# Performance work log

Measured on AMD Instinct MI355X. Metric: run time of the kernel, lower is better.

Reference implementation:

```python
import jax, jax.numpy as jnp
import numpy as np

T, B, H = 512, 128, 512


def setup_inputs() -> dict:
    key = jax.random.key(0)
    k1, k2, k3, k4 = jax.random.split(key, 4)
    scale_i = 1.0 / np.sqrt(H)
    return {
        "ins": jax.random.normal(k1, (T, B, H), dtype=jnp.float32),
        "resets": jax.random.randint(k2, (T, B), 0, 2).astype(bool),
        "h0": jnp.zeros((B, H), dtype=jnp.float32),
        "W_i": jax.random.normal(k3, (H, 3 * H), dtype=jnp.float32) * scale_i,
        "b_i": jnp.zeros((3 * H,), dtype=jnp.float32),
        "W_h": jax.random.normal(k4, (H, 3 * H), dtype=jnp.float32) * scale_i,
        "b_hn": jnp.zeros((H,), dtype=jnp.float32),
    }


def reference(ins, resets, h0, W_i, b_i, W_h, b_hn):
    # Precompute all input-side gate projections in one big GEMM: [T,B,3H]
    gi = jnp.einsum('tbh,hk->tbk', ins, W_i) + b_i

    def step(h, inp):
        gi_t, r_t = inp  # gi_t: [B,3H], r_t: [B] bool
        # episode reset -> zero carry (flax initialize_carry default is zeros)
        h = jnp.where(r_t[:, None], 0.0, h)
        gh = h @ W_h  # [B,3H]
        ir, iz, inn = jnp.split(gi_t, 3, axis=-1)
        hr, hz, hn = jnp.split(gh, 3, axis=-1)
        r = jax.nn.sigmoid(ir + hr)
        z = jax.nn.sigmoid(iz + hz)
        n = jnp.tanh(inn + r * (hn + b_hn))
        new_h = (1.0 - z) * n + z * h
        return new_h, new_h

    final_h, ys = jax.lax.scan(step, h0, (gi, resets))
    return final_h, ys  # carry [B,H], outputs [T,B,H]
```

## Files before the change

### kernel.cpp

```cpp
#include <hip/hip_runtime.h>
#include <stdint.h>
#include <math.h>

#define T_DIM 512
#define B_DIM 128
#define H_DIM 512
#define K_MAX_SWEEP 32

typedef _Float16 half8 __attribute__((ext_vector_type(8)));
typedef float    f32x4 __attribute__((ext_vector_type(4)));

__global__ void k_weights(const float* __restrict__ Wi, const float* __restrict__ Wh,
                          _Float16* __restrict__ Bsw) {
    __shared__ float sh[32][33];
    int nt = blockIdx.x;
    int kt = blockIdx.y;
    int m  = blockIdx.z;
    const float* W = m ? Wh : Wi;
    int ty = threadIdx.x >> 5, tx = threadIdx.x & 31;
    for (int i = 0; i < 4; ++i) {
        int r = ty + i * 8;
        sh[r][tx] = W[(kt * 32 + r) * 1536 + nt * 32 + tx];
    }
    __syncthreads();
    for (int i = 0; i < 4; ++i) {
        int nloc  = ty + i * 8;
        int nglob = nt * 32 + nloc;
        float v   = sh[tx][nloc];
        int kglob = kt * 32 + tx;
        int np, kp;
        if (m == 0) { np = nglob;                                  kp = kglob;       }
        else        { np = (nglob < 1024) ? nglob : nglob + 512;   kp = 512 + kglob; }
        Bsw[np * 1024 + kp] = (_Float16)v;
    }
}

__global__ void k_xcast(const float* __restrict__ ins, _Float16* __restrict__ Acomb) {
    size_t i   = (size_t)blockIdx.x * blockDim.x + threadIdx.x;
    size_t row = i >> 6;
    int    c8  = (int)(i & 63);
    const float4* s = (const float4*)(ins + row * 512 + c8 * 8);
    float4 a = s[0], b = s[1];
    half8 hv;
    hv[0] = (_Float16)a.x; hv[1] = (_Float16)a.y; hv[2] = (_Float16)a.z; hv[3] = (_Float16)a.w;
    hv[4] = (_Float16)b.x; hv[5] = (_Float16)b.y; hv[6] = (_Float16)b.z; hv[7] = (_Float16)b.w;
    *(half8*)(Acomb + row * 1024 + c8 * 8) = hv;
}

__global__ void k_age(const uint8_t* __restrict__ resets, uint16_t* __restrict__ age,
                      int* __restrict__ hist2d) {
    int b = blockIdx.x;
    int t = threadIdx.x;
    __shared__ int sAny;
    __shared__ int sh[512];
    __shared__ int hist[512];
    if (t == 0) sAny = 0;
    hist[t] = 0;
    __syncthreads();
    if ((t & 3) && resets[t]) atomicOr(&sAny, 1);
    __syncthreads();
    bool is_i32 = (sAny == 0);
    int idx = t * B_DIM + b;
    int r;
    if (is_i32) r = (((const int*)resets)[idx] != 0);
    else        r = (resets[idx] != 0);
    sh[t] = r ? t : 0;
    __syncthreads();
    for (int off = 1; off < 512; off <<= 1) {
        int v = (t >= off) ? sh[t - off] : 0;
        __syncthreads();
        if (v > sh[t]) sh[t] = v;
        __syncthreads();
    }
    int a = t - sh[t];
    age[idx] = (uint16_t)a;
    atomicAdd(&hist[a], 1);
    __syncthreads();
    hist2d[b * 512 + t] = hist[t];
}

__global__ void k_prefix(const int* __restrict__ hist2d, int* __restrict__ cnt,
                         int* __restrict__ offs, int* __restrict__ cur) {
    int a = threadIdx.x;
    int s = 0;
    for (int b = 0; b < 128; ++b) s += hist2d[b * 512 + a];
    __shared__ int sh[512];
    sh[a] = s;
    __syncthreads();
    for (int off = 1; off < 512; off <<= 1) {
        int v = (a >= off) ? sh[a - off] : 0;
        __syncthreads();
        sh[a] += v;
        __syncthreads();
    }
    cnt[a]  = s;
    offs[a] = sh[a] - s;
    cur[a]  = sh[a] - s;
}

__global__ void k_scatter(const uint16_t* __restrict__ age, int* __restrict__ cur,
                          int* __restrict__ rows) {
    int b = blockIdx.x;
    int t = threadIdx.x;
    __shared__ int lcnt[512];
    __shared__ int lbase[512];
    lcnt[t] = 0;
    __syncthreads();
    int a  = age[t * B_DIM + b];
    int li = atomicAdd(&lcnt[a], 1);
    __syncthreads();
    if (lcnt[t] > 0) lbase[t] = atomicAdd(&cur[t], lcnt[t]);
    __syncthreads();
    rows[lbase[a] + li] = t * B_DIM + b;
}

template <bool F16A>
__launch_bounds__(256, 4)
__global__ void k_sweep(const float* __restrict__ ins, const _Float16* __restrict__ Bsw,
                        _Float16* __restrict__ Acomb, const int* __restrict__ rows,
                        const int* __restrict__ cnt, const int* __restrict__ offs,
                        const float* __restrict__ b_i, const float* __restrict__ b_hn,
                        float* __restrict__ out, int sweep) {
    int nrows    = cnt[sweep];
    int tileBase = blockIdx.y * 128;
    if (tileBase >= nrows) return;
    int cgi  = blockIdx.x;
    int off0 = offs[sweep];
    float* ys = out + B_DIM * H_DIM;

    __shared__ int rowsL[128];
    __shared__ __align__(16) _Float16 As[128][64];
    __shared__ __align__(16) _Float16 Bs[3][32][64];

    int tid = threadIdx.x;
    if (tid < 128) {
        int gi = tileBase + tid;
        rowsL[tid] = rows[off0 + ((gi < nrows) ? gi : 0)];
    }
    __syncthreads();

    f32x4 acc[2][8];
    for (int i = 0; i < 2; ++i)
        for (int j = 0; j < 8; ++j) acc[i][j] = (f32x4){0.f, 0.f, 0.f, 0.f};

    const int kIters = (sweep == 0) ? 8 : 16;
    int w = tid >> 6, lane = tid & 63, q = lane >> 4, l15 = lane & 15;
    int w32 = w * 32;
    int lr = tid >> 1, c0 = (tid & 1) * 4, rs = lr & 7;
    int brow = tid >> 3, bch = tid & 7, brs = brow & 7;
    int la = l15 & 7;

    for (int it = 0; it < kIters; ++it) {
        int  kw    = it * 64;
        bool xpart = (kw < 512);
        if (F16A) {
            const uint4* s = (const uint4*)(Acomb + (size_t)rowsL[lr] * 1024 + kw + c0 * 8);
            uint4 v0 = s[0], v1 = s[1], v2 = s[2], v3 = s[3];
            *(uint4*)&As[lr][((c0 + 0) ^ rs) << 3] = v0;
            *(uint4*)&As[lr][((c0 + 1) ^ rs) << 3] = v1;
            *(uint4*)&As[lr][((c0 + 2) ^ rs) << 3] = v2;
            *(uint4*)&As[lr][((c0 + 3) ^ rs) << 3] = v3;
        } else {
            int rowidx = rowsL[lr];
            const float* src = xpart ? (ins + (size_t)rowidx * 512 + kw)
                                     : (ys + (size_t)(rowidx - 128) * 512 + (kw - 512));
            const float4* s4 = (const float4*)(src + c0 * 8);
            float4 v[8];
            #pragma unroll
            for (int j = 0; j < 8; ++j) v[j] = s4[j];
            #pragma unroll
            for (int c = 0; c < 4; ++c) {
                float4 a = v[c * 2], b2 = v[c * 2 + 1];
                half8 hv;
                hv[0] = (_Float16)a.x;  hv[1] = (_Float16)a.y;
                hv[2] = (_Float16)a.z;  hv[3] = (_Float16)a.w;
                hv[4] = (_Float16)b2.x; hv[5] = (_Float16)b2.y;
                hv[6] = (_Float16)b2.z; hv[7] = (_Float16)b2.w;
                *(half8*)&As[lr][((c0 + c) ^ rs) << 3] = hv;
            }
        }
        {
            int nbs[3];
            nbs[0] = cgi * 32;
            nbs[1] = 512 + cgi * 32;
            nbs[2] = (xpart ? 1024 : 1536) + cgi * 32;
            #pragma unroll
            for (int s = 0; s < 3; ++s) {
                const uint4* g = (const uint4*)(Bsw + (nbs[s] + brow) * 1024 + kw + bch * 8);
                *(uint4*)&Bs[s][brow][(bch ^ brs) << 3] = *g;
            }
        }
        __syncthreads();
        #pragma unroll
        for (int ks = 0; ks < 2; ++ks) {
            int ca = ks * 4 + q;
            int sc = (ca ^ la) << 3;
            half8 a0  = *(const half8*)&As[w32 + l15][sc];
            half8 a1  = *(const half8*)&As[w32 + 16 + l15][sc];
            half8 b00 = *(const half8*)&Bs[0][l15][sc];
            half8 b01 = *(const half8*)&Bs[0][16 + l15][sc];
            half8 b10 = *(const half8*)&Bs[1][l15][sc];
            half8 b11 = *(const half8*)&Bs[1][16 + l15][sc];
            half8 b20 = *(const half8*)&Bs[2][l15][sc];
            half8 b21 = *(const half8*)&Bs[2][16 + l15][sc];
            acc[0][0] = __builtin_amdgcn_mfma_f32_16x16x32_f16(a0, b00, acc[0][0], 0, 0, 0);
            acc[1][0] = __builtin_amdgcn_mfma_f32_16x16x32_f16(a1, b00, acc[1][0], 0, 0, 0);
            acc[0][1] = __builtin_amdgcn_mfma_f32_16x16x32_f16(a0, b01, acc[0][1], 0, 0, 0);
            acc[1][1] = __builtin_amdgcn_mfma_f32_16x16x32_f16(a1, b01, acc[1][1], 0, 0, 0);
            acc[0][2] = __builtin_amdgcn_mfma_f32_16x16x32_f16(a0, b10, acc[0][2], 0, 0, 0);
            acc[1][2] = __builtin_amdgcn_mfma_f32_16x16x32_f16(a1, b10, acc[1][2], 0, 0, 0);
            acc[0][3] = __builtin_amdgcn_mfma_f32_16x16x32_f16(a0, b11, acc[0][3], 0, 0, 0);
            acc[1][3] = __builtin_amdgcn_mfma_f32_16x16x32_f16(a1, b11, acc[1][3], 0, 0, 0);
            if (xpart) {
                acc[0][4] = __builtin_amdgcn_mfma_f32_16x16x32_f16(a0, b20, acc[0][4], 0, 0, 0);
                acc[1][4] = __builtin_amdgcn_mfma_f32_16x16x32_f16(a1, b20, acc[1][4], 0, 0, 0);
                acc[0][5] = __builtin_amdgcn_mfma_f32_16x16x32_f16(a0, b21, acc[0][5], 0, 0, 0);
                acc[1][5] = __builtin_amdgcn_mfma_f32_16x16x32_f16(a1, b21, acc[1][5], 0, 0, 0);
            } else {
                acc[0][6] = __builtin_amdgcn_mfma_f32_16x16x32_f16(a0, b20, acc[0][6], 0, 0, 0);
                acc[1][6] = __builtin_amdgcn_mfma_f32_16x16x32_f16(a1, b20, acc[1][6], 0, 0, 0);
                acc[0][7] = __builtin_amdgcn_mfma_f32_16x16x32_f16(a0, b21, acc[0][7], 0, 0, 0);
                acc[1][7] = __builtin_amdgcn_mfma_f32_16x16x32_f16(a1, b21, acc[1][7], 0, 0, 0);
            }
        }
        __syncthreads();
    }

    #pragma unroll
    for (int tm = 0; tm < 2; ++tm) {
        int lrow_base = w32 + tm * 16 + q * 4;
        #pragma unroll
        for (int reg = 0; reg < 4; ++reg) {
            int lrow = lrow_base + reg;
            if (tileBase + lrow >= nrows) continue;
            int rowidx = rowsL[lrow];
            int t = rowidx >> 7, b = rowidx & 127;
            #pragma unroll
            for (int hf = 0; hf < 2; ++hf) {
                int gj = cgi * 32 + hf * 16 + l15;
                float rpre = acc[tm][0 + hf][reg] + b_i[gj];
                float zpre = acc[tm][2 + hf][reg] + b_i[512 + gj];
                float innv = acc[tm][4 + hf][reg] + b_i[1024 + gj];
                float hnv  = acc[tm][6 + hf][reg];
                float r = 1.f / (1.f + __expf(-rpre));
                float z = 1.f / (1.f + __expf(-zpre));
                float n = tanhf(innv + r * (hnv + b_hn[gj]));
                float hprev = (sweep > 0) ? ys[(size_t)(rowidx - 128) * 512 + gj] : 0.f;
                float hnew  = (1.f - z) * n + z * hprev;
                ys[(size_t)rowidx * 512 + gj] = hnew;
                if (F16A && rowidx + 128 < T_DIM * B_DIM)
                    Acomb[(size_t)(rowidx + 128) * 1024 + 512 + gj] = (_Float16)hnew;
                if (t == T_DIM - 1) out[b * 512 + gj] = hnew;
            }
        }
    }
}

__global__ void k_cleanup(const float* __restrict__ ins, const _Float16* __restrict__ Bsw,
                          const int* __restrict__ rows, const int* __restrict__ cnt,
                          const int* __restrict__ offs, const float* __restrict__ b_i,
                          const float* __restrict__ b_hn, float* __restrict__ out) {
    float* ys = out + B_DIM * H_DIM;
    __shared__ float xs[512], hs[512];
    int j = threadIdx.x;
    for (int a = K_MAX_SWEEP; a < 512; ++a) {
        int n = cnt[a];
        if (n == 0) return;
        int o = offs[a];
        for (int i = 0; i < n; ++i) {
            int rowidx = rows[o + i];
            xs[j] = ins[rowidx * 512 + j];
            hs[j] = ys[(rowidx - 128) * 512 + j];
            __syncthreads();
            float rpre = b_i[j], zpre = b_i[512 + j], innv = b_i[1024 + j], hnv = 0.f;
            for (int k = 0; k < 512; ++k) {
                float xk = xs[k], hk = hs[k];
                rpre += xk * (float)Bsw[j * 1024 + k]          + hk * (float)Bsw[j * 1024 + 512 + k];
                zpre += xk * (float)Bsw[(512 + j) * 1024 + k]  + hk * (float)Bsw[(512 + j) * 1024 + 512 + k];
                innv += xk * (float)Bsw[(1024 + j) * 1024 + k];
                hnv  += hk * (float)Bsw[(1536 + j) * 1024 + 512 + k];
            }
            float r  = 1.f / (1.f + __expf(-rpre));
            float z  = 1.f / (1.f + __expf(-zpre));
            float nn = tanhf(innv + r * (hnv + b_hn[j]));
            float hnew = (1.f - z) * nn + z * hs[j];
            ys[rowidx * 512 + j] = hnew;
            int t = rowidx >> 7, b = rowidx & 127;
            if (t == 511) out[b * 512 + j] = hnew;
            __syncthreads();
        }
    }
}

extern "C" void kernel_launch(void* const* d_in, const int* in_sizes, int n_in,
                              void* d_out, int out_size, void* d_ws, size_t ws_size,
                              hipStream_t stream) {
    const float*   ins    = (const float*)d_in[0];
    const uint8_t* resets = (const uint8_t*)d_in[1];
    const float*   Wi     = (const float*)d_in[3];
    const float*   b_i    = (const float*)d_in[4];
    const float*   Wh     = (const float*)d_in[5];
    const float*   b_hn   = (const float*)d_in[6];
    float*         out    = (float*)d_out;

    const size_t BSW_B   = 2048ull * 1024 * 2;
    const size_t ACOMB_B = 65536ull * 1024 * 2;
    const size_t TAIL_B  = 131072 + 262144 + 3 * 2048 + 262144;
    char* ws = (char*)d_ws;
    size_t off = 0;
    _Float16* Bsw = (_Float16*)(ws + off); off += BSW_B;
    bool big = (ws_size >= BSW_B + ACOMB_B + TAIL_B);
    _Float16* Acomb = nullptr;
    if (big) { Acomb = (_Float16*)(ws + off); off += ACOMB_B; }
    uint16_t* age    = (uint16_t*)(ws + off); off += 131072;
    int*      hist2d = (int*)(ws + off);      off += 262144;
    int*      cnt    = (int*)(ws + off);      off += 2048;
    int*      offs   = (int*)(ws + off);      off += 2048;
    int*      cur    = (int*)(ws + off);      off += 2048;
    int*      rows   = (int*)(ws + off);      off += 262144;

    k_weights<<<dim3(48, 16, 2), dim3(256), 0, stream>>>(Wi, Wh, Bsw);
    if (big)
        k_xcast<<<dim3(16384), dim3(256), 0, stream>>>(ins, Acomb);
    k_age    <<<dim3(128), dim3(512), 0, stream>>>(resets, age, hist2d);
    k_prefix <<<dim3(1),   dim3(512), 0, stream>>>(hist2d, cnt, offs, cur);
    k_scatter<<<dim3(128), dim3(512), 0, stream>>>(age, cur, rows);

    for (int k = 0; k < K_MAX_SWEEP; ++k) {
        int tiles = 512 / (k + 1) + 1;
        if (tiles > 512) tiles = 512;
        if (big)
            k_sweep<true><<<dim3(16, tiles), dim3(256), 0, stream>>>(ins, Bsw, Acomb, rows, cnt,
                                                                     offs, b_i, b_hn, out, k);
        else
            k_sweep<false><<<dim3(16, tiles), dim3(256), 0, stream>>>(ins, Bsw, Acomb, rows, cnt,
                                                                      offs, b_i, b_hn, out, k);
    }
    k_cleanup<<<dim3(1), dim3(512), 0, stream>>>(ins, Bsw, rows, cnt, offs, b_i, b_hn, out);
}
```

Before: 936.9 us.

## Replace per-sweep launches and serial cleanup with persistent grid-barrier tail kernel

Only the first three age sweeps now get their own kernel launches. All later ages, including the former single-block serial cleanup for ages of 32 and above, are handled by one persistent kernel of 512 blocks. That kernel loops over ages, splits each age's tiles across its blocks, and separates ages with an atomic grid-wide barrier. This removes many small launches and the slow serial cleanup, but it relies on all 512 blocks being resident at once and pays a barrier cost for every remaining age.

```diff
diff --git a/kernel.cpp b/kernel.cpp
--- a/kernel.cpp
+++ b/kernel.cpp
@@ -5,7 +5,8 @@
 #define T_DIM 512
 #define B_DIM 128
 #define H_DIM 512
-#define K_MAX_SWEEP 32
+#define KSTART_TAIL 3
+#define TOTAL_ROWS (T_DIM * B_DIM)
 
 typedef _Float16 half8 __attribute__((ext_vector_type(8)));
 typedef float    f32x4 __attribute__((ext_vector_type(4)));
@@ -80,8 +81,10 @@
 }
 
 __global__ void k_prefix(const int* __restrict__ hist2d, int* __restrict__ cnt,
-                         int* __restrict__ offs, int* __restrict__ cur) {
+                         int* __restrict__ offs, int* __restrict__ cur,
+                         int* __restrict__ bar) {
     int a = threadIdx.x;
+    if (a == 0) bar[0] = 0;
     int s = 0;
     for (int b = 0; b < 128; ++b) s += hist2d[b * 512 + a];
     __shared__ int sh[512];
@@ -115,24 +118,16 @@
 }
 
 template <bool F16A>
-__launch_bounds__(256, 4)
-__global__ void k_sweep(const float* __restrict__ ins, const _Float16* __restrict__ Bsw,
-                        _Float16* __restrict__ Acomb, const int* __restrict__ rows,
-                        const int* __restrict__ cnt, const int* __restrict__ offs,
-                        const float* __restrict__ b_i, const float* __restrict__ b_hn,
-                        float* __restrict__ out, int sweep) {
-    int nrows    = cnt[sweep];
-    int tileBase = blockIdx.y * 128;
-    if (tileBase >= nrows) return;
-    int cgi  = blockIdx.x;
-    int off0 = offs[sweep];
-    float* ys = out + B_DIM * H_DIM;
-
-    __shared__ int rowsL[128];
-    __shared__ __align__(16) _Float16 As[128][64];
-    __shared__ __align__(16) _Float16 Bs[3][32][64];
-
+__device__ __forceinline__ void sweep_tile(
+    int sweep, int cgi, int tileBase, int nrows, int off0,
+    const float* __restrict__ ins, const _Float16* __restrict__ Bsw,
+    _Float16* __restrict__ Acomb, const int* __restrict__ rows,
+    const float* __restrict__ b_i, const float* __restrict__ b_hn,
+    float* __restrict__ out, float* __restrict__ ys,
+    int (&rowsL)[128], _Float16 (&As)[128][64], _Float16 (&Bs)[3][32][64])
+{
     int tid = threadIdx.x;
+    __syncthreads();
     if (tid < 128) {
         int gi = tileBase + tid;
         rowsL[tid] = rows[off0 + ((gi < nrows) ? gi : 0)];
@@ -248,7 +243,7 @@
                 float hprev = (sweep > 0) ? ys[(size_t)(rowidx - 128) * 512 + gj] : 0.f;
                 float hnew  = (1.f - z) * n + z * hprev;
                 ys[(size_t)rowidx * 512 + gj] = hnew;
-                if (F16A && rowidx + 128 < T_DIM * B_DIM)
+                if (F16A && rowidx + 128 < TOTAL_ROWS)
                     Acomb[(size_t)(rowidx + 128) * 1024 + 512 + gj] = (_Float16)hnew;
                 if (t == T_DIM - 1) out[b * 512 + gj] = hnew;
             }
@@ -256,39 +251,64 @@
     }
 }
 
-__global__ void k_cleanup(const float* __restrict__ ins, const _Float16* __restrict__ Bsw,
-                          const int* __restrict__ rows, const int* __restrict__ cnt,
-                          const int* __restrict__ offs, const float* __restrict__ b_i,
-                          const float* __restrict__ b_hn, float* __restrict__ out) {
+template <bool F16A>
+__launch_bounds__(256, 4)
+__global__ void k_sweep(const float* __restrict__ ins, const _Float16* __restrict__ Bsw,
+                        _Float16* __restrict__ Acomb, const int* __restrict__ rows,
+                        const int* __restrict__ cnt, const int* __restrict__ offs,
+                        const float* __restrict__ b_i, const float* __restrict__ b_hn,
+                        float* __restrict__ out, int sweep) {
+    int nrows    = cnt[sweep];
+    int tileBase = blockIdx.y * 128;
+    if (tileBase >= nrows) return;
+    __shared__ int rowsL[128];
+    __shared__ __align__(16) _Float16 As[128][64];
+    __shared__ __align__(16) _Float16 Bs[3][32][64];
     float* ys = out + B_DIM * H_DIM;
-    __shared__ float xs[512], hs[512];
-    int j = threadIdx.x;
-    for (int a = K_MAX_SWEEP; a < 512; ++a) {
-        int n = cnt[a];
-        if (n == 0) return;
-        int o = offs[a];
-        for (int i = 0; i < n; ++i) {
-            int rowidx = rows[o + i];
-            xs[j] = ins[rowidx * 512 + j];
-            hs[j] = ys[(rowidx - 128) * 512 + j];
-            __syncthreads();
-            float rpre = b_i[j], zpre = b_i[512 + j], innv = b_i[1024 + j], hnv = 0.f;
-            for (int k = 0; k < 512; ++k) {
-                float xk = xs[k], hk = hs[k];
-                rpre += xk * (float)Bsw[j * 1024 + k]          + hk * (float)Bsw[j * 1024 + 512 + k];
-                zpre += xk * (float)Bsw[(512 + j) * 1024 + k]  + hk * (float)Bsw[(512 + j) * 1024 + 512 + k];
-                innv += xk * (float)Bsw[(1024 + j) * 1024 + k];
-                hnv  += hk * (float)Bsw[(1536 + j) * 1024 + 512 + k];
-            }
-            float r  = 1.f / (1.f + __expf(-rpre));
-            float z  = 1.f / (1.f + __expf(-zpre));
-            float nn = tanhf(innv + r * (hnv + b_hn[j]));
-            float hnew = (1.f - z) * nn + z * hs[j];
-            ys[rowidx * 512 + j] = hnew;
-            int t = rowidx >> 7, b = rowidx & 127;
-            if (t == 511) out[b * 512 + j] = hnew;
-            __syncthreads();
-        }
+    sweep_tile<F16A>(sweep, blockIdx.x, tileBase, nrows, offs[sweep],
+                     ins, Bsw, Acomb, rows, b_i, b_hn, out, ys, rowsL, As, Bs);
+}
+
+template <bool F16A>
+__launch_bounds__(256, 4)
+__global__ void k_tail(const float* __restrict__ ins, const _Float16* __restrict__ Bsw,
+                       _Float16* __restrict__ Acomb, const int* __restrict__ rows,
+                       const int* __restrict__ cnt, const int* __restrict__ offs,
+                       const float* __restrict__ b_i, const float* __restrict__ b_hn,
+                       float* __restrict__ out, int kstart, int* bar) {
+    __shared__ int rowsL[128];
+    __shared__ __align__(16) _Float16 As[128][64];
+    __shared__ __align__(16) _Float16 Bs[3][32][64];
+    float* ys = out + B_DIM * H_DIM;
+    int tid = threadIdx.x;
+    int phase = 0;
+    const int nblk = (int)gridDim.x;
+
+    for (int k = kstart; k < 512; ++k) {
+        int done = offs[k];
+        if (done >= TOTAL_ROWS) break;
+        int nrows = cnt[k];
+        if (nrows > 0) {
+            int nwork = (((nrows + 127) >> 7) << 4);
+            for (int wi = blockIdx.x; wi < nwork; wi += nblk) {
+                int cgi = wi & 15;
+                int tb  = (wi >> 4) << 7;
+                sweep_tile<F16A>(k, cgi, tb, nrows, done,
+                                 ins, Bsw, Acomb, rows, b_i, b_hn, out, ys,
+                                 rowsL, As, Bs);
+            }
+        }
+        ++phase;
+        __syncthreads();
+        if (tid == 0) {
+            __threadfence();
+            __hip_atomic_fetch_add(bar, 1, __ATOMIC_RELEASE, __HIP_MEMORY_SCOPE_AGENT);
+            while (__hip_atomic_load(bar, __ATOMIC_ACQUIRE, __HIP_MEMORY_SCOPE_AGENT)
+                   < phase * nblk) {
+                __builtin_amdgcn_s_sleep(2);
+            }
+        }
+        __syncthreads();
     }
 }
 
@@ -305,7 +325,7 @@
 
     const size_t BSW_B   = 2048ull * 1024 * 2;
     const size_t ACOMB_B = 65536ull * 1024 * 2;
-    const size_t TAIL_B  = 131072 + 262144 + 3 * 2048 + 262144;
+    const size_t TAIL_B  = 131072 + 262144 + 3 * 2048 + 262144 + 64;
     char* ws = (char*)d_ws;
     size_t off = 0;
     _Float16* Bsw = (_Float16*)(ws + off); off += BSW_B;
@@ -318,15 +338,16 @@
     int*      offs   = (int*)(ws + off);      off += 2048;
     int*      cur    = (int*)(ws + off);      off += 2048;
     int*      rows   = (int*)(ws + off);      off += 262144;
+    int*      bar    = (int*)(ws + off);      off += 64;
 
     k_weights<<<dim3(48, 16, 2), dim3(256), 0, stream>>>(Wi, Wh, Bsw);
     if (big)
         k_xcast<<<dim3(16384), dim3(256), 0, stream>>>(ins, Acomb);
     k_age    <<<dim3(128), dim3(512), 0, stream>>>(resets, age, hist2d);
-    k_prefix <<<dim3(1),   dim3(512), 0, stream>>>(hist2d, cnt, offs, cur);
+    k_prefix <<<dim3(1),   dim3(512), 0, stream>>>(hist2d, cnt, offs, cur, bar);
     k_scatter<<<dim3(128), dim3(512), 0, stream>>>(age, cur, rows);
 
-    for (int k = 0; k < K_MAX_SWEEP; ++k) {
+    for (int k = 0; k < KSTART_TAIL; ++k) {
         int tiles = 512 / (k + 1) + 1;
         if (tiles > 512) tiles = 512;
         if (big)
@@ -336,5 +357,10 @@
             k_sweep<false><<<dim3(16, tiles), dim3(256), 0, stream>>>(ins, Bsw, Acomb, rows, cnt,
                                                                       offs, b_i, b_hn, out, k);
     }
-    k_cleanup<<<dim3(1), dim3(512), 0, stream>>>(ins, Bsw, rows, cnt, offs, b_i, b_hn, out);
-}
+    if (big)
+        k_tail<true><<<dim3(512), dim3(256), 0, stream>>>(ins, Bsw, Acomb, rows, cnt, offs,
+                                                          b_i, b_hn, out, KSTART_TAIL, bar);
+    else
+        k_tail<false><<<dim3(512), dim3(256), 0, stream>>>(ins, Bsw, Acomb, rows, cnt, offs,
+                                                           b_i, b_hn, out, KSTART_TAIL, bar);
+}
```

After: 2.825 ms. +201.5%, slower.

## Precompute input gates in one GEMM and run tail sweeps in a persistent kernel

Applied to the files above, without the earlier changes.

Adds k_gi, which computes all input-side gate projections in one full GEMM over every row. It finishes age-0 rows directly and stores the other rows' gate pre-activations as fp16 in a new gi2 buffer. Each sweep then only multiplies against W_h, with K halved. Sweeps from age 3 onward run in a single persistent 256-block kernel that uses an atomic grid barrier between ages, replacing the per-age launches and the serial single-block cleanup. This needs a large extra workspace, adds a spin-barrier that assumes all blocks are co-resident, and rounds the gate pre-activations to fp16.

```diff
diff --git a/kernel.cpp b/kernel.cpp
--- a/kernel.cpp
+++ b/kernel.cpp
@@ -5,7 +5,9 @@
 #define T_DIM 512
 #define B_DIM 128
 #define H_DIM 512
+#define KSTART_TAIL 3
 #define K_MAX_SWEEP 32
+#define TOTAL_ROWS (T_DIM * B_DIM)
 
 typedef _Float16 half8 __attribute__((ext_vector_type(8)));
 typedef float    f32x4 __attribute__((ext_vector_type(4)));
@@ -80,8 +82,10 @@
 }
 
 __global__ void k_prefix(const int* __restrict__ hist2d, int* __restrict__ cnt,
-                         int* __restrict__ offs, int* __restrict__ cur) {
+                         int* __restrict__ offs, int* __restrict__ cur,
+                         int* __restrict__ bar) {
     int a = threadIdx.x;
+    if (a == 0) bar[0] = 0;
     int s = 0;
     for (int b = 0; b < 128; ++b) s += hist2d[b * 512 + a];
     __shared__ int sh[512];
@@ -112,6 +116,253 @@
     if (lcnt[t] > 0) lbase[t] = atomicAdd(&cur[t], lcnt[t]);
     __syncthreads();
     rows[lbase[a] + li] = t * B_DIM + b;
+}
+
+
+__launch_bounds__(256, 4)
+__global__ void k_gi(const _Float16* __restrict__ AcombC, _Float16* __restrict__ Acomb,
+                     const _Float16* __restrict__ Bsw, const uint16_t* __restrict__ age,
+                     const float* __restrict__ b_i, const float* __restrict__ b_hn,
+                     float* __restrict__ out, _Float16* __restrict__ gi2) {
+    int cgi     = blockIdx.x;
+    int rowbase = blockIdx.y * 128;
+    float* ys = out + B_DIM * H_DIM;
+
+    __shared__ __align__(16) _Float16 As[128][64];
+    __shared__ __align__(16) _Float16 Bs[3][32][64];
+
+    int tid = threadIdx.x;
+    f32x4 acc[2][6];
+    for (int i = 0; i < 2; ++i)
+        for (int j = 0; j < 6; ++j) acc[i][j] = (f32x4){0.f, 0.f, 0.f, 0.f};
+
+    int w = tid >> 6, lane = tid & 63, q = lane >> 4, l15 = lane & 15;
+    int w32 = w * 32;
+    int lr = tid >> 1, c0 = (tid & 1) * 4, rs = lr & 7;
+    int brow = tid >> 3, bch = tid & 7, brs = brow & 7;
+    int la = l15 & 7;
+
+    for (int it = 0; it < 8; ++it) {
+        int kw = it * 64;
+        {
+            const uint4* s = (const uint4*)(AcombC + (size_t)(rowbase + lr) * 1024 + kw + c0 * 8);
+            uint4 v0 = s[0], v1 = s[1], v2 = s[2], v3 = s[3];
+            *(uint4*)&As[lr][((c0 + 0) ^ rs) << 3] = v0;
+            *(uint4*)&As[lr][((c0 + 1) ^ rs) << 3] = v1;
+            *(uint4*)&As[lr][((c0 + 2) ^ rs) << 3] = v2;
+            *(uint4*)&As[lr][((c0 + 3) ^ rs) << 3] = v3;
+        }
+        {
+            int nbs[3] = { cgi * 32, 512 + cgi * 32, 1024 + cgi * 32 };
+            #pragma unroll
+            for (int s = 0; s < 3; ++s) {
+                const uint4* g = (const uint4*)(Bsw + (nbs[s] + brow) * 1024 + kw + bch * 8);
+                *(uint4*)&Bs[s][brow][(bch ^ brs) << 3] = *g;
+            }
+        }
+        __syncthreads();
+        #pragma unroll
+        for (int ks = 0; ks < 2; ++ks) {
+            int ca = ks * 4 + q;
+            int sc = (ca ^ la) << 3;
+            half8 a0 = *(const half8*)&As[w32 + l15][sc];
+            half8 a1 = *(const half8*)&As[w32 + 16 + l15][sc];
+            #pragma unroll
+            for (int s = 0; s < 3; ++s) {
+                half8 b0 = *(const half8*)&Bs[s][l15][sc];
+                half8 b1 = *(const half8*)&Bs[s][16 + l15][sc];
+                acc[0][s*2+0] = __builtin_amdgcn_mfma_f32_16x16x32_f16(a0, b0, acc[0][s*2+0], 0, 0, 0);
+                acc[1][s*2+0] = __builtin_amdgcn_mfma_f32_16x16x32_f16(a1, b0, acc[1][s*2+0], 0, 0, 0);
+                acc[0][s*2+1] = __builtin_amdgcn_mfma_f32_16x16x32_f16(a0, b1, acc[0][s*2+1], 0, 0, 0);
+                acc[1][s*2+1] = __builtin_amdgcn_mfma_f32_16x16x32_f16(a1, b1, acc[1][s*2+1], 0, 0, 0);
+            }
+        }
+        __syncthreads();
+    }
+
+    #pragma unroll
+    for (int tm = 0; tm < 2; ++tm) {
+        #pragma unroll
+        for (int reg = 0; reg < 4; ++reg) {
+            int lrow = w32 + tm * 16 + q * 4 + reg;
+            int row  = rowbase + lrow;
+            int t = row >> 7, b = row & 127;
+            int a = age[row];
+            #pragma unroll
+            for (int hf = 0; hf < 2; ++hf) {
+                int gj = cgi * 32 + hf * 16 + l15;
+                float rpre = acc[tm][0 + hf][reg] + b_i[gj];
+                float zpre = acc[tm][2 + hf][reg] + b_i[512 + gj];
+                float innv = acc[tm][4 + hf][reg] + b_i[1024 + gj];
+                if (a == 0) {
+                    float r = 1.f / (1.f + __expf(-rpre));
+                    float z = 1.f / (1.f + __expf(-zpre));
+                    float n = tanhf(innv + r * b_hn[gj]);
+                    float hnew = (1.f - z) * n;
+                    ys[(size_t)row * 512 + gj] = hnew;
+                    if (row + 128 < TOTAL_ROWS)
+                        Acomb[(size_t)(row + 128) * 1024 + 512 + gj] = (_Float16)hnew;
+                    if (t == T_DIM - 1) out[b * 512 + gj] = hnew;
+                } else {
+                    size_t gb = ((size_t)cgi * TOTAL_ROWS + row) * 96 + hf * 16 + l15;
+                    gi2[gb]      = (_Float16)rpre;
+                    gi2[gb + 32] = (_Float16)zpre;
+                    gi2[gb + 64] = (_Float16)innv;
+                }
+            }
+        }
+    }
+}
+
+__device__ __forceinline__ void sweep_h_tile(
+    int cgi, int tileBase, int nrows, int off0,
+    _Float16* __restrict__ Acomb, const _Float16* __restrict__ Bsw,
+    const int* __restrict__ rows, const _Float16* __restrict__ gi2,
+    const float* __restrict__ b_hn, float* __restrict__ out, float* __restrict__ ys,
+    int (&rowsL)[128], _Float16 (&As)[128][64], _Float16 (&Bs)[3][32][64])
+{
+    int tid = threadIdx.x;
+    __syncthreads();
+    if (tid < 128) {
+        int gi = tileBase + tid;
+        rowsL[tid] = rows[off0 + ((gi < nrows) ? gi : 0)];
+    }
+    __syncthreads();
+
+    f32x4 acc[2][6];
+    for (int i = 0; i < 2; ++i)
+        for (int j = 0; j < 6; ++j) acc[i][j] = (f32x4){0.f, 0.f, 0.f, 0.f};
+
+    int w = tid >> 6, lane = tid & 63, q = lane >> 4, l15 = lane & 15;
+    int w32 = w * 32;
+    int lr = tid >> 1, c0 = (tid & 1) * 4, rs = lr & 7;
+    int brow = tid >> 3, bch = tid & 7, brs = brow & 7;
+    int la = l15 & 7;
+
+    for (int it = 0; it < 8; ++it) {
+        int kw = it * 64;
+        {
+            const uint4* s = (const uint4*)(Acomb + (size_t)rowsL[lr] * 1024 + 512 + kw + c0 * 8);
+            uint4 v0 = s[0], v1 = s[1], v2 = s[2], v3 = s[3];
+            *(uint4*)&As[lr][((c0 + 0) ^ rs) << 3] = v0;
+            *(uint4*)&As[lr][((c0 + 1) ^ rs) << 3] = v1;
+            *(uint4*)&As[lr][((c0 + 2) ^ rs) << 3] = v2;
+            *(uint4*)&As[lr][((c0 + 3) ^ rs) << 3] = v3;
+        }
+        {
+            int nbs[3] = { cgi * 32, 512 + cgi * 32, 1536 + cgi * 32 };
+            #pragma unroll
+            for (int s = 0; s < 3; ++s) {
+                const uint4* g = (const uint4*)(Bsw + (nbs[s] + brow) * 1024 + 512 + kw + bch * 8);
+                *(uint4*)&Bs[s][brow][(bch ^ brs) << 3] = *g;
+            }
+        }
+        __syncthreads();
+        #pragma unroll
+        for (int ks = 0; ks < 2; ++ks) {
+            int ca = ks * 4 + q;
+            int sc = (ca ^ la) << 3;
+            half8 a0 = *(const half8*)&As[w32 + l15][sc];
+            half8 a1 = *(const half8*)&As[w32 + 16 + l15][sc];
+            #pragma unroll
+            for (int s = 0; s < 3; ++s) {
+                half8 b0 = *(const half8*)&Bs[s][l15][sc];
+                half8 b1 = *(const half8*)&Bs[s][16 + l15][sc];
+                acc[0][s*2+0] = __builtin_amdgcn_mfma_f32_16x16x32_f16(a0, b0, acc[0][s*2+0], 0, 0, 0);
+                acc[1][s*2+0] = __builtin_amdgcn_mfma_f32_16x16x32_f16(a1, b0, acc[1][s*2+0], 0, 0, 0);
+                acc[0][s*2+1] = __builtin_amdgcn_mfma_f32_16x16x32_f16(a0, b1, acc[0][s*2+1], 0, 0, 0);
+                acc[1][s*2+1] = __builtin_amdgcn_mfma_f32_16x16x32_f16(a1, b1, acc[1][s*2+1], 0, 0, 0);
+            }
+        }
+        __syncthreads();
+    }
+
+    #pragma unroll
+    for (int tm = 0; tm < 2; ++tm) {
+        #pragma unroll
+        for (int reg = 0; reg < 4; ++reg) {
+            int lrow = w32 + tm * 16 + q * 4 + reg;
+            if (tileBase + lrow >= nrows) continue;
+            int row = rowsL[lrow];
+            int t = row >> 7, b = row & 127;
+            #pragma unroll
+            for (int hf = 0; hf < 2; ++hf) {
+                int gj = cgi * 32 + hf * 16 + l15;
+                size_t gb = ((size_t)cgi * TOTAL_ROWS + row) * 96 + hf * 16 + l15;
+                float gr  = (float)gi2[gb];
+                float gz  = (float)gi2[gb + 32];
+                float gin = (float)gi2[gb + 64];
+                float rpre = acc[tm][0 + hf][reg] + gr;
+                float zpre = acc[tm][2 + hf][reg] + gz;
+                float r = 1.f / (1.f + __expf(-rpre));
+                float z = 1.f / (1.f + __expf(-zpre));
+                float n = tanhf(gin + r * (acc[tm][4 + hf][reg] + b_hn[gj]));
+                float hprev = ys[(size_t)(row - 128) * 512 + gj];
+                float hnew  = (1.f - z) * n + z * hprev;
+                ys[(size_t)row * 512 + gj] = hnew;
+                if (row + 128 < TOTAL_ROWS)
+                    Acomb[(size_t)(row + 128) * 1024 + 512 + gj] = (_Float16)hnew;
+                if (t == T_DIM - 1) out[b * 512 + gj] = hnew;
+            }
+        }
+    }
+}
+
+__launch_bounds__(256, 4)
+__global__ void k_sweep_h(_Float16* __restrict__ Acomb, const _Float16* __restrict__ Bsw,
+                          const int* __restrict__ rows, const int* __restrict__ cnt,
+                          const int* __restrict__ offs, const _Float16* __restrict__ gi2,
+                          const float* __restrict__ b_hn, float* __restrict__ out, int sweep) {
+    int nrows    = cnt[sweep];
+    int tileBase = blockIdx.y * 128;
+    if (tileBase >= nrows) return;
+    __shared__ int rowsL[128];
+    __shared__ __align__(16) _Float16 As[128][64];
+    __shared__ __align__(16) _Float16 Bs[3][32][64];
+    float* ys = out + B_DIM * H_DIM;
+    sweep_h_tile(blockIdx.x, tileBase, nrows, offs[sweep],
+                 Acomb, Bsw, rows, gi2, b_hn, out, ys, rowsL, As, Bs);
+}
+
+__launch_bounds__(256, 4)
+__global__ void k_tail_h(_Float16* __restrict__ Acomb, const _Float16* __restrict__ Bsw,
+                         const int* __restrict__ rows, const int* __restrict__ cnt,
+                         const int* __restrict__ offs, const _Float16* __restrict__ gi2,
+                         const float* __restrict__ b_hn, float* __restrict__ out,
+                         int kstart, int* bar) {
+    __shared__ int rowsL[128];
+    __shared__ __align__(16) _Float16 As[128][64];
+    __shared__ __align__(16) _Float16 Bs[3][32][64];
+    float* ys = out + B_DIM * H_DIM;
+    int tid = threadIdx.x;
+    int phase = 0;
+    const int nblk = (int)gridDim.x;
+
+    for (int k = kstart; k < 512; ++k) {
+        int done = offs[k];
+        if (done >= TOTAL_ROWS) break;
+        int nrows = cnt[k];
+        if (nrows > 0) {
+            int nwork = (((nrows + 127) >> 7) << 4);
+            for (int wi = blockIdx.x; wi < nwork; wi += nblk) {
+                int cgi = wi & 15;
+                int tb  = (wi >> 4) << 7;
+                sweep_h_tile(cgi, tb, nrows, done,
+                             Acomb, Bsw, rows, gi2, b_hn, out, ys, rowsL, As, Bs);
+            }
+        }
+        ++phase;
+        __syncthreads();
+        if (tid == 0) {
+            __hip_atomic_fetch_add(bar, 1, __ATOMIC_RELEASE, __HIP_MEMORY_SCOPE_AGENT);
+            while (__hip_atomic_load(bar, __ATOMIC_RELAXED, __HIP_MEMORY_SCOPE_AGENT)
+                   < phase * nblk) {
+                __builtin_amdgcn_s_sleep(4);
+            }
+            __builtin_amdgcn_fence(__ATOMIC_ACQUIRE, "agent");
+        }
+        __syncthreads();
+    }
 }
 
 template <bool F16A>
@@ -248,7 +499,7 @@
                 float hprev = (sweep > 0) ? ys[(size_t)(rowidx - 128) * 512 + gj] : 0.f;
                 float hnew  = (1.f - z) * n + z * hprev;
                 ys[(size_t)rowidx * 512 + gj] = hnew;
-                if (F16A && rowidx + 128 < T_DIM * B_DIM)
+                if (F16A && rowidx + 128 < TOTAL_ROWS)
                     Acomb[(size_t)(rowidx + 128) * 1024 + 512 + gj] = (_Float16)hnew;
                 if (t == T_DIM - 1) out[b * 512 + gj] = hnew;
             }
@@ -305,36 +556,54 @@
 
     const size_t BSW_B   = 2048ull * 1024 * 2;
     const size_t ACOMB_B = 65536ull * 1024 * 2;
-    const size_t TAIL_B  = 131072 + 262144 + 3 * 2048 + 262144;
+    const size_t GI2_B   = 16ull * TOTAL_ROWS * 96 * 2;
+    const size_t FIXED_B = 131072 + 262144 + 3 * 2048 + 262144 + 64;
+
     char* ws = (char*)d_ws;
     size_t off = 0;
-    _Float16* Bsw = (_Float16*)(ws + off); off += BSW_B;
-    bool big = (ws_size >= BSW_B + ACOMB_B + TAIL_B);
-    _Float16* Acomb = nullptr;
-    if (big) { Acomb = (_Float16*)(ws + off); off += ACOMB_B; }
+    _Float16* Bsw    = (_Float16*)(ws + off); off += BSW_B;
     uint16_t* age    = (uint16_t*)(ws + off); off += 131072;
     int*      hist2d = (int*)(ws + off);      off += 262144;
     int*      cnt    = (int*)(ws + off);      off += 2048;
     int*      offs   = (int*)(ws + off);      off += 2048;
     int*      cur    = (int*)(ws + off);      off += 2048;
     int*      rows   = (int*)(ws + off);      off += 262144;
+    int*      bar    = (int*)(ws + off);      off += 64;
+
+    bool big      = (ws_size >= BSW_B + FIXED_B + ACOMB_B);
+    bool new_path = (ws_size >= BSW_B + FIXED_B + ACOMB_B + GI2_B);
+    _Float16* Acomb = nullptr;
+    _Float16* gi2   = nullptr;
+    if (big)      { Acomb = (_Float16*)(ws + off); off += ACOMB_B; }
+    if (new_path) { gi2   = (_Float16*)(ws + off); off += GI2_B;   }
 
     k_weights<<<dim3(48, 16, 2), dim3(256), 0, stream>>>(Wi, Wh, Bsw);
     if (big)
         k_xcast<<<dim3(16384), dim3(256), 0, stream>>>(ins, Acomb);
     k_age    <<<dim3(128), dim3(512), 0, stream>>>(resets, age, hist2d);
-    k_prefix <<<dim3(1),   dim3(512), 0, stream>>>(hist2d, cnt, offs, cur);
+    k_prefix <<<dim3(1),   dim3(512), 0, stream>>>(hist2d, cnt, offs, cur, bar);
     k_scatter<<<dim3(128), dim3(512), 0, stream>>>(age, cur, rows);
 
-    for (int k = 0; k < K_MAX_SWEEP; ++k) {
-        int tiles = 512 / (k + 1) + 1;
-        if (tiles > 512) tiles = 512;
-        if (big)
-            k_sweep<true><<<dim3(16, tiles), dim3(256), 0, stream>>>(ins, Bsw, Acomb, rows, cnt,
-                                                                     offs, b_i, b_hn, out, k);
-        else
-            k_sweep<false><<<dim3(16, tiles), dim3(256), 0, stream>>>(ins, Bsw, Acomb, rows, cnt,
-                                                                      offs, b_i, b_hn, out, k);
-    }
-    k_cleanup<<<dim3(1), dim3(512), 0, stream>>>(ins, Bsw, rows, cnt, offs, b_i, b_hn, out);
-}
+    if (new_path) {
+        k_gi<<<dim3(16, 512), dim3(256), 0, stream>>>(Acomb, Acomb, Bsw, age, b_i, b_hn, out, gi2);
+        for (int k = 1; k < KSTART_TAIL; ++k) {
+            int tiles = 512 / (k + 1) + 1;
+            k_sweep_h<<<dim3(16, tiles), dim3(256), 0, stream>>>(Acomb, Bsw, rows, cnt, offs,
+                                                                 gi2, b_hn, out, k);
+        }
+        k_tail_h<<<dim3(256), dim3(256), 0, stream>>>(Acomb, Bsw, rows, cnt, offs,
+                                                      gi2, b_hn, out, KSTART_TAIL, bar);
+    } else {
+        for (int k = 0; k < K_MAX_SWEEP; ++k) {
+            int tiles = 512 / (k + 1) + 1;
+            if (tiles > 512) tiles = 512;
+            if (big)
+                k_sweep<true><<<dim3(16, tiles), dim3(256), 0, stream>>>(ins, Bsw, Acomb, rows,
+                                                                         cnt, offs, b_i, b_hn, out, k);
+            else
+                k_sweep<false><<<dim3(16, tiles), dim3(256), 0, stream>>>(ins, Bsw, Acomb, rows,
+                                                                          cnt, offs, b_i, b_hn, out, k);
+        }
+        k_cleanup<<<dim3(1), dim3(512), 0, stream>>>(ins, Bsw, rows, cnt, offs, b_i, b_hn, out);
+    }
+}
```

Result: slower. 1.059 ms (+13.0%).
